# Optimization experiments

Measured on AMD Instinct MI355X. Metric: run time of the kernel, lower is better.

The kernel has to match this reference:

```python
import jax, jax.numpy as jnp
import numpy as np

SEQ, BATCH, D_IN, HIDDEN = 2048, 64, 512, 512


def setup_inputs() -> dict:
    key = jax.random.key(0)
    k_x, k_wi, k_wh = jax.random.split(key, 3)
    scale_in = 1.0 / np.sqrt(D_IN)      # ~lecun_normal fan_in
    scale_h = 1.0 / np.sqrt(HIDDEN)
    return {
        "x": jax.random.normal(k_x, (SEQ, BATCH, D_IN), dtype=jnp.float32),
        "c0": jnp.zeros((BATCH, HIDDEN), dtype=jnp.float32),
        "h0": jnp.zeros((BATCH, HIDDEN), dtype=jnp.float32),
        "Wi": jax.random.normal(k_wi, (D_IN, 4 * HIDDEN), dtype=jnp.float32) * scale_in,
        "Wh": jax.random.normal(k_wh, (HIDDEN, 4 * HIDDEN), dtype=jnp.float32) * scale_h,
        "b": jnp.zeros((4 * HIDDEN,), dtype=jnp.float32),
    }


def reference(x, c0, h0, Wi, Wh, b):
    # flax LSTMCell scanned over the leading (time) axis.
    # Gate order: i, f, g, o. Input projection has no bias in flax;
    # hidden projection carries the bias -> combined into single b.
    def step(carry, xt):
        c, h = carry
        z = xt @ Wi + h @ Wh + b            # [B, 4H]
        i, f, g, o = jnp.split(z, 4, axis=-1)
        i = jax.nn.sigmoid(i)
        f = jax.nn.sigmoid(f)
        g = jnp.tanh(g)
        o = jax.nn.sigmoid(o)
        c_new = f * c + i * g
        h_new = o * jnp.tanh(c_new)
        return (c_new, h_new), h_new

    (cT, hT), ys = jax.lax.scan(step, (c0, h0), x)
    return cT, hT, ys  # final carry + stacked hidden states [S, B, H]
```

## Files before the change

kernel.cpp:

```cpp
#include <hip/hip_runtime.h>

#define SEQ    2048
#define BATCH  64
#define DIN    512
#define HID    512
#define GATES  2048
#define NB     64
#define NT     256
#define TC     8
#define ZST    33

typedef short bf16v8 __attribute__((ext_vector_type(8)));
typedef float f32x4  __attribute__((ext_vector_type(4)));

static __device__ __forceinline__ unsigned short f2bfbits(float f) {
    union { __bf16 h; unsigned short s; } u;
    u.h = (__bf16)f;
    return u.s;
}

static __device__ __forceinline__ bf16v8 cvt8(const float* __restrict__ p) {
    float4 a = *(const float4*)(p);
    float4 b = *(const float4*)(p + 4);
    union { __bf16 h[8]; bf16v8 v; } u;
    u.h[0] = (__bf16)a.x; u.h[1] = (__bf16)a.y;
    u.h[2] = (__bf16)a.z; u.h[3] = (__bf16)a.w;
    u.h[4] = (__bf16)b.x; u.h[5] = (__bf16)b.y;
    u.h[6] = (__bf16)b.z; u.h[7] = (__bf16)b.w;
    return u.v;
}

static __device__ __forceinline__ float sigm(float v) {
    return 1.0f / (1.0f + __expf(-v));
}
static __device__ __forceinline__ float ftanh(float v) {
    return 1.0f - 2.0f / (__expf(2.0f * v) + 1.0f);
}

__global__ void __launch_bounds__(NT, 1) lstm_fused(
    const float* __restrict__ x,  const float* __restrict__ c0,
    const float* __restrict__ h0, const float* __restrict__ Wi,
    const float* __restrict__ Wh, const float* __restrict__ bias,
    float* __restrict__ out, unsigned int* slots, unsigned short* hws)
{
    __shared__ unsigned short wi_lds[32 * 512];
    __shared__ unsigned short wh_lds[32 * 512];
    __shared__ float zxb[TC * 64 * ZST];
    __shared__ unsigned short hxch[64 * 8];

    const int tid   = threadIdx.x;
    const int blk   = blockIdx.x;
    const int lane  = tid & 63;
    const int wv    = tid >> 6;
    const int col   = lane & 15;
    const int rgrp  = lane >> 4;
    const int c7    = col & 7;
    const int hbase = blk * 8;

    for (int idx = tid; idx < 32 * 512; idx += NT) {
        const int c = idx & 31;
        const int k = idx >> 5;
        const int gc = (c >> 3) * HID + hbase + (c & 7);
        const int sidx = c * 512 + ((((k >> 3) ^ (c & 7)) << 3) | (k & 7));
        wi_lds[sidx] = f2bfbits(Wi[(size_t)k * GATES + gc]);
        wh_lds[sidx] = f2bfbits(Wh[(size_t)k * GATES + gc]);
    }

    unsigned short* hb0 = hws;
    unsigned short* hb1 = hws + 64 * 64 * 8;
    for (int idx = blk * NT + tid; idx < 64 * 64 * 8; idx += NB * NT) {
        const int kb = idx >> 9, row = (idx >> 3) & 63, j = idx & 7;
        __hip_atomic_store(&hb0[idx], f2bfbits(h0[row * HID + kb * 8 + j]),
                           __ATOMIC_RELAXED, __HIP_MEMORY_SCOPE_AGENT);
    }

    __syncthreads();
    if (tid == 0)
        __hip_atomic_store(&slots[blk << 4], 1u,
                           __ATOMIC_RELAXED, __HIP_MEMORY_SCOPE_AGENT);
    if (wv == 1) {
        unsigned int v;
        do {
            v = __hip_atomic_load(&slots[lane << 4],
                                  __ATOMIC_RELAXED, __HIP_MEMORY_SCOPE_AGENT);
        } while (!__all(v >= 1u));
    }
    __syncthreads();

    const int brow_a = wv * 16 + col;
    const int hcol   = hbase + col;
    const float bv0 = bias[(col >> 3) * HID + hbase + c7];
    const float bv1 = bias[((col + 16) >> 3) * HID + hbase + c7];

    float cv[4];
    #pragma unroll
    for (int r = 0; r < 4; ++r) {
        const int brow = wv * 16 + rgrp * 4 + r;
        cv[r] = (col < 8) ? c0[brow * HID + hcol] : 0.0f;
    }

    const size_t YS = 2 * (size_t)BATCH * HID;

    for (int t0 = 0; t0 < SEQ; t0 += TC) {
        for (int m = wv; m < (TC * 64) >> 4; m += 4) {
            const float* xtile = x + ((size_t)t0 * 64 + m * 16 + col) * DIN;
            f32x4 a0 = {0.f, 0.f, 0.f, 0.f};
            f32x4 a1 = {0.f, 0.f, 0.f, 0.f};
            #pragma unroll
            for (int ks = 0; ks < 16; ++ks) {
                const int kofs = ks * 32 + rgrp * 8;
                bf16v8 axv = cvt8(xtile + kofs);
                const int gsw = (((ks * 4 + rgrp) ^ c7) << 3);
                bf16v8 b0 = *(const bf16v8*)(wi_lds + col * 512 + gsw);
                bf16v8 b1 = *(const bf16v8*)(wi_lds + (col + 16) * 512 + gsw);
                a0 = __builtin_amdgcn_mfma_f32_16x16x32_bf16(axv, b0, a0, 0, 0, 0);
                a1 = __builtin_amdgcn_mfma_f32_16x16x32_bf16(axv, b1, a1, 0, 0, 0);
            }
            #pragma unroll
            for (int r = 0; r < 4; ++r) {
                const int row = m * 16 + rgrp * 4 + r;
                zxb[row * ZST + col]      = a0[r] + bv0;
                zxb[row * ZST + col + 16] = a1[r] + bv1;
            }
        }
        __syncthreads();

        for (int tt = 0; tt < TC; ++tt) {
            const int t = t0 + tt;
            const unsigned int kk = (unsigned int)t + 2u;
            const unsigned short* hr = (t & 1) ? hb1 : hb0;
            unsigned short*       hw = (t & 1) ? hb0 : hb1;

            unsigned long long hq0[16], hq1[16];
            {
                const unsigned long long* hsrc = (const unsigned long long*)hr;
                #pragma unroll
                for (int ks = 0; ks < 16; ++ks) {
                    const int kblk = ks * 4 + rgrp;
                    const unsigned long long* p =
                        hsrc + ((size_t)(kblk * 64 + brow_a) << 1);
                    hq0[ks] = __hip_atomic_load(p, __ATOMIC_RELAXED,
                                                __HIP_MEMORY_SCOPE_AGENT);
                    hq1[ks] = __hip_atomic_load(p + 1, __ATOMIC_RELAXED,
                                                __HIP_MEMORY_SCOPE_AGENT);
                }
            }

            f32x4 acc0, acc1;
            #pragma unroll
            for (int r = 0; r < 4; ++r) {
                const int row = tt * 64 + wv * 16 + rgrp * 4 + r;
                acc0[r] = zxb[row * ZST + col];
                acc1[r] = zxb[row * ZST + col + 16];
            }

            #pragma unroll
            for (int ks = 0; ks < 16; ++ks) {
                union { unsigned long long q[2]; bf16v8 v; } hu;
                hu.q[0] = hq0[ks];
                hu.q[1] = hq1[ks];
                const int gsw = (((ks * 4 + rgrp) ^ c7) << 3);
                bf16v8 b0 = *(const bf16v8*)(wh_lds + col * 512 + gsw);
                bf16v8 b1 = *(const bf16v8*)(wh_lds + (col + 16) * 512 + gsw);
                acc0 = __builtin_amdgcn_mfma_f32_16x16x32_bf16(hu.v, b0, acc0, 0, 0, 0);
                acc1 = __builtin_amdgcn_mfma_f32_16x16x32_bf16(hu.v, b1, acc1, 0, 0, 0);
            }

            float zf[4], zo[4];
            #pragma unroll
            for (int r = 0; r < 4; ++r) {
                zf[r] = __shfl_xor(acc0[r], 8);
                zo[r] = __shfl_xor(acc1[r], 8);
            }

            float hn[4], cnl[4];
            if (col < 8) {
                #pragma unroll
                for (int r = 0; r < 4; ++r) {
                    const float ig = sigm(acc0[r]);
                    const float fg = sigm(zf[r]);
                    const float gg = ftanh(acc1[r]);
                    const float og = sigm(zo[r]);
                    const float cn = fg * cv[r] + ig * gg;
                    cv[r] = cn;
                    cnl[r] = cn;
                    hn[r] = og * ftanh(cn);
                    const int brow = wv * 16 + rgrp * 4 + r;
                    hxch[brow * 8 + c7] = f2bfbits(hn[r]);
                }
            }
            __syncthreads();

            if (wv == 0) {
                const unsigned long long* sp =
                    (const unsigned long long*)(hxch + lane * 8);
                unsigned long long e0 = sp[0], e1 = sp[1];
                unsigned long long* dst = (unsigned long long*)
                    (hw + (((size_t)blk * 64 + lane) << 3));
                __hip_atomic_store(dst, e0, __ATOMIC_RELAXED,
                                   __HIP_MEMORY_SCOPE_AGENT);
                __hip_atomic_store(dst + 1, e1, __ATOMIC_RELAXED,
                                   __HIP_MEMORY_SCOPE_AGENT);
                asm volatile("s_waitcnt vmcnt(0)" ::: "memory");
                if (lane == 0)
                    __hip_atomic_store(&slots[blk << 4], kk,
                                       __ATOMIC_RELAXED,
                                       __HIP_MEMORY_SCOPE_AGENT);
            }

            if (col < 8) {
                #pragma unroll
                for (int r = 0; r < 4; ++r) {
                    const int brow = wv * 16 + rgrp * 4 + r;
                    out[YS + ((size_t)t * BATCH + brow) * HID + hcol] = hn[r];
                    if (t == SEQ - 1) {
                        out[(size_t)brow * HID + hcol] = cnl[r];
                        out[(size_t)BATCH * HID + brow * HID + hcol] = hn[r];
                    }
                }
            }

            if (wv == 1) {
                unsigned int v;
                do {
                    v = __hip_atomic_load(&slots[lane << 4],
                                          __ATOMIC_RELAXED,
                                          __HIP_MEMORY_SCOPE_AGENT);
                } while (!__all(v >= kk));
            }
            __syncthreads();
        }
    }
}

extern "C" void kernel_launch(void* const* d_in, const int* in_sizes, int n_in,
                              void* d_out, int out_size, void* d_ws, size_t ws_size,
                              hipStream_t stream) {
    const float* x  = (const float*)d_in[0];
    const float* c0 = (const float*)d_in[1];
    const float* h0 = (const float*)d_in[2];
    const float* Wi = (const float*)d_in[3];
    const float* Wh = (const float*)d_in[4];
    const float* b  = (const float*)d_in[5];
    float* out = (float*)d_out;

    char* wsb = (char*)d_ws;
    unsigned int* slots = (unsigned int*)wsb;
    unsigned short* hws = (unsigned short*)(wsb + 4096);

    hipMemsetAsync(slots, 0, 4096, stream);

    lstm_fused<<<dim3(NB), dim3(NT), 0, stream>>>(
        x, c0, h0, Wi, Wh, b, out, slots, hws);
}
```

Before: 24.94 ms.

## Tag hidden-state words with step version to replace barrier-based cross-block sync

Adds a new persistent LSTM kernel in which each bf16 hidden value is packed with a 16-bit timestep tag into a 32-bit word and written to double-buffered global memory. Consumers spin directly on the tagged data instead of waiting on a global arrival counter, so the per-step grid barrier leaves the critical path. A relaxed slot counter still keeps writers from overwriting a buffer before every block has read it. The cost is twice the global traffic per hidden value, a larger workspace, and more polling loads. The old kernel is kept as a fallback when the workspace is too small.

```diff
diff --git a/kernel.cpp b/kernel.cpp
--- a/kernel.cpp
+++ b/kernel.cpp
@@ -37,7 +37,226 @@
     return 1.0f - 2.0f / (__expf(2.0f * v) + 1.0f);
 }
 
-__global__ void __launch_bounds__(NT, 1) lstm_fused(
+__global__ void __launch_bounds__(NT, 1) lstm_v6(
+    const float* __restrict__ x,  const float* __restrict__ c0,
+    const float* __restrict__ h0, const float* __restrict__ Wi,
+    const float* __restrict__ Wh, const float* __restrict__ bias,
+    float* __restrict__ out, unsigned int* slots, unsigned int* htag)
+{
+    __shared__ unsigned short wi_lds[32 * 512];
+    __shared__ unsigned short wh_lds[32 * 512];
+    __shared__ float zxb[TC * 64 * ZST];
+    __shared__ unsigned int hx[64 * 8];
+
+    const int tid   = threadIdx.x;
+    const int blk   = blockIdx.x;
+    const int lane  = tid & 63;
+    const int wv    = tid >> 6;
+    const int col   = lane & 15;
+    const int rgrp  = lane >> 4;
+    const int c7    = col & 7;
+    const int hbase = blk * 8;
+
+    for (int idx = tid; idx < 32 * 512; idx += NT) {
+        const int c = idx & 31;
+        const int k = idx >> 5;
+        const int gc = (c >> 3) * HID + hbase + (c & 7);
+        const int sidx = c * 512 + ((((k >> 3) ^ (c & 7)) << 3) | (k & 7));
+        wi_lds[sidx] = f2bfbits(Wi[(size_t)k * GATES + gc]);
+        wh_lds[sidx] = f2bfbits(Wh[(size_t)k * GATES + gc]);
+    }
+
+    unsigned int* hb0 = htag;
+    unsigned int* hb1 = htag + 32768;
+    for (int idx = blk * NT + tid; idx < 32768; idx += NB * NT) {
+        const int kb = idx >> 9, row = (idx >> 3) & 63, j = idx & 7;
+        const unsigned int w =
+            ((unsigned int)f2bfbits(h0[row * HID + kb * 8 + j]) << 16) | 1u;
+        __hip_atomic_store(&hb1[idx], w,
+                           __ATOMIC_RELAXED, __HIP_MEMORY_SCOPE_AGENT);
+    }
+
+    const int brow_a = wv * 16 + col;
+    const int hcol   = hbase + col;
+    const float bv0 = bias[(col >> 3) * HID + hbase + c7];
+    const float bv1 = bias[((col + 16) >> 3) * HID + hbase + c7];
+
+    float cv[4];
+    #pragma unroll
+    for (int r = 0; r < 4; ++r) {
+        const int brow = wv * 16 + rgrp * 4 + r;
+        cv[r] = (col < 8) ? c0[brow * HID + hcol] : 0.0f;
+    }
+
+    const size_t YS = 2 * (size_t)BATCH * HID;
+
+    for (int t0 = 0; t0 < SEQ; t0 += TC) {
+        for (int m = wv; m < (TC * 64) >> 4; m += 4) {
+            const float* xtile = x + ((size_t)t0 * 64 + m * 16 + col) * DIN;
+            f32x4 a0 = {0.f, 0.f, 0.f, 0.f};
+            f32x4 a1 = {0.f, 0.f, 0.f, 0.f};
+            #pragma unroll
+            for (int ks = 0; ks < 16; ++ks) {
+                const int kofs = ks * 32 + rgrp * 8;
+                bf16v8 axv = cvt8(xtile + kofs);
+                const int gsw = (((ks * 4 + rgrp) ^ c7) << 3);
+                bf16v8 b0 = *(const bf16v8*)(wi_lds + col * 512 + gsw);
+                bf16v8 b1 = *(const bf16v8*)(wi_lds + (col + 16) * 512 + gsw);
+                a0 = __builtin_amdgcn_mfma_f32_16x16x32_bf16(axv, b0, a0, 0, 0, 0);
+                a1 = __builtin_amdgcn_mfma_f32_16x16x32_bf16(axv, b1, a1, 0, 0, 0);
+            }
+            #pragma unroll
+            for (int r = 0; r < 4; ++r) {
+                const int row = m * 16 + rgrp * 4 + r;
+                zxb[row * ZST + col]      = a0[r] + bv0;
+                zxb[row * ZST + col + 16] = a1[r] + bv1;
+            }
+        }
+        __syncthreads();
+
+        for (int tt = 0; tt < TC; ++tt) {
+            const int t = t0 + tt;
+            const unsigned int vin  = (unsigned int)t + 1u;
+            const unsigned int texp = vin & 0xffffu;
+            const unsigned int wtag = (vin + 1u) & 0xffffu;
+            const unsigned int* hr  = (vin & 1u) ? hb1 : hb0;
+            unsigned int*       hwt = (vin & 1u) ? hb0 : hb1;
+
+            unsigned int gv = 0;
+            if (wv == 0)
+                gv = __hip_atomic_load(&slots[lane << 4],
+                                       __ATOMIC_RELAXED, __HIP_MEMORY_SCOPE_AGENT);
+
+            unsigned int pa[16][4];
+            #pragma unroll
+            for (int hf = 0; hf < 2; ++hf) {
+                unsigned long long q[32];
+                const int ksb = hf * 8;
+                #pragma unroll
+                for (int k2 = 0; k2 < 8; ++k2) {
+                    const unsigned long long* p = (const unsigned long long*)hr
+                        + ((size_t)(((ksb + k2) * 4 + rgrp) * 64 + brow_a) << 2);
+                    #pragma unroll
+                    for (int j = 0; j < 4; ++j)
+                        q[k2 * 4 + j] = __hip_atomic_load(p + j,
+                            __ATOMIC_RELAXED, __HIP_MEMORY_SCOPE_AGENT);
+                }
+                while (true) {
+                    bool ok = true;
+                    #pragma unroll
+                    for (int i = 0; i < 32; ++i)
+                        ok = ok && (((unsigned int)q[i] & 0xffffu) == texp)
+                                && (((unsigned int)(q[i] >> 32) & 0xffffu) == texp);
+                    if (ok) break;
+                    __builtin_amdgcn_s_sleep(1);
+                    #pragma unroll
+                    for (int k2 = 0; k2 < 8; ++k2) {
+                        const unsigned long long* p = (const unsigned long long*)hr
+                            + ((size_t)(((ksb + k2) * 4 + rgrp) * 64 + brow_a) << 2);
+                        #pragma unroll
+                        for (int j = 0; j < 4; ++j)
+                            q[k2 * 4 + j] = __hip_atomic_load(p + j,
+                                __ATOMIC_RELAXED, __HIP_MEMORY_SCOPE_AGENT);
+                    }
+                }
+                #pragma unroll
+                for (int k2 = 0; k2 < 8; ++k2)
+                    #pragma unroll
+                    for (int j = 0; j < 4; ++j) {
+                        const unsigned long long qq = q[k2 * 4 + j];
+                        pa[ksb + k2][j] =
+                            ((unsigned int)(qq >> 32) & 0xffff0000u) |
+                            ((unsigned int)qq >> 16);
+                    }
+            }
+
+            __syncthreads();
+            if (tid == 0)
+                __hip_atomic_store(&slots[blk << 4], vin,
+                                   __ATOMIC_RELAXED, __HIP_MEMORY_SCOPE_AGENT);
+
+            f32x4 acc0, acc1;
+            #pragma unroll
+            for (int r = 0; r < 4; ++r) {
+                const int row = tt * 64 + wv * 16 + rgrp * 4 + r;
+                acc0[r] = zxb[row * ZST + col];
+                acc1[r] = zxb[row * ZST + col + 16];
+            }
+
+            #pragma unroll
+            for (int ks = 0; ks < 16; ++ks) {
+                union { unsigned int w[4]; bf16v8 v; } hu;
+                hu.w[0] = pa[ks][0]; hu.w[1] = pa[ks][1];
+                hu.w[2] = pa[ks][2]; hu.w[3] = pa[ks][3];
+                const int gsw = (((ks * 4 + rgrp) ^ c7) << 3);
+                bf16v8 b0 = *(const bf16v8*)(wh_lds + col * 512 + gsw);
+                bf16v8 b1 = *(const bf16v8*)(wh_lds + (col + 16) * 512 + gsw);
+                acc0 = __builtin_amdgcn_mfma_f32_16x16x32_bf16(hu.v, b0, acc0, 0, 0, 0);
+                acc1 = __builtin_amdgcn_mfma_f32_16x16x32_bf16(hu.v, b1, acc1, 0, 0, 0);
+            }
+
+            float zf[4], zo[4];
+            #pragma unroll
+            for (int r = 0; r < 4; ++r) {
+                zf[r] = __shfl_xor(acc0[r], 8);
+                zo[r] = __shfl_xor(acc1[r], 8);
+            }
+
+            float hn[4], cnl[4];
+            if (col < 8) {
+                #pragma unroll
+                for (int r = 0; r < 4; ++r) {
+                    const float ig = sigm(acc0[r]);
+                    const float fg = sigm(zf[r]);
+                    const float gg = ftanh(acc1[r]);
+                    const float og = sigm(zo[r]);
+                    const float cn = fg * cv[r] + ig * gg;
+                    cv[r] = cn;
+                    cnl[r] = cn;
+                    hn[r] = og * ftanh(cn);
+                    const int brow = wv * 16 + rgrp * 4 + r;
+                    hx[brow * 8 + c7] =
+                        ((unsigned int)f2bfbits(hn[r]) << 16) | wtag;
+                }
+            }
+            __syncthreads();
+
+            if (wv == 0) {
+                while (!__all(gv >= vin)) {
+                    __builtin_amdgcn_s_sleep(1);
+                    gv = __hip_atomic_load(&slots[lane << 4],
+                                           __ATOMIC_RELAXED,
+                                           __HIP_MEMORY_SCOPE_AGENT);
+                }
+                const unsigned int* sp = hx + lane * 8;
+                unsigned long long* dst = (unsigned long long*)hwt
+                    + ((size_t)(blk * 64 + lane) << 2);
+                #pragma unroll
+                for (int j = 0; j < 4; ++j) {
+                    const unsigned long long e =
+                        (unsigned long long)sp[2 * j] |
+                        ((unsigned long long)sp[2 * j + 1] << 32);
+                    __hip_atomic_store(dst + j, e,
+                                       __ATOMIC_RELAXED, __HIP_MEMORY_SCOPE_AGENT);
+                }
+            }
+
+            if (col < 8) {
+                #pragma unroll
+                for (int r = 0; r < 4; ++r) {
+                    const int brow = wv * 16 + rgrp * 4 + r;
+                    out[YS + ((size_t)t * BATCH + brow) * HID + hcol] = hn[r];
+                    if (t == SEQ - 1) {
+                        out[(size_t)brow * HID + hcol] = cnl[r];
+                        out[(size_t)BATCH * HID + brow * HID + hcol] = hn[r];
+                    }
+                }
+            }
+        }
+    }
+}
+
+__global__ void __launch_bounds__(NT, 1) lstm_v5(
     const float* __restrict__ x,  const float* __restrict__ c0,
     const float* __restrict__ h0, const float* __restrict__ Wi,
     const float* __restrict__ Wh, const float* __restrict__ bias,
@@ -246,10 +465,17 @@
 
     char* wsb = (char*)d_ws;
     unsigned int* slots = (unsigned int*)wsb;
-    unsigned short* hws = (unsigned short*)(wsb + 4096);
-
-    hipMemsetAsync(slots, 0, 4096, stream);
-
-    lstm_fused<<<dim3(NB), dim3(NT), 0, stream>>>(
-        x, c0, h0, Wi, Wh, b, out, slots, hws);
-}
+
+    const size_t v6_need = 4096 + 2ull * 32768 * sizeof(unsigned int);
+    if (ws_size >= v6_need) {
+        unsigned int* htag = (unsigned int*)(wsb + 4096);
+        hipMemsetAsync(wsb, 0, v6_need, stream);
+        lstm_v6<<<dim3(NB), dim3(NT), 0, stream>>>(
+            x, c0, h0, Wi, Wh, b, out, slots, htag);
+    } else {
+        unsigned short* hws = (unsigned short*)(wsb + 4096);
+        hipMemsetAsync(slots, 0, 4096, stream);
+        lstm_v5<<<dim3(NB), dim3(NT), 0, stream>>>(
+            x, c0, h0, Wi, Wh, b, out, slots, hws);
+    }
+}
```

Result: slower. 37.85 ms (+51.8%).
